# Performance work log

Measured on AMD Instinct MI355X. Metric: run time of the kernel, lower is better.

## Reference

```python
import jax, jax.numpy as jnp
import numpy as np

D_MODEL = 1024
D_STATE = 16
D_CONV = 4
EXPAND = 2
D_INNER = EXPAND * D_MODEL          # 2048
DT_RANK = D_MODEL // 16             # 64
B, L = 2, 1024
LN_EPS = 1e-5


def setup_inputs() -> dict:
    key = jax.random.key(0)
    ks = jax.random.split(key, 8)
    s = lambda k, shape, sc: jax.random.normal(k, shape, jnp.float32) * sc
    inp = {
        'x': jax.random.normal(ks[0], (B, L, D_MODEL), jnp.float32),
        'ln_w': jnp.ones((D_MODEL,), jnp.float32),
        'ln_b': jnp.zeros((D_MODEL,), jnp.float32),
        'W_in': s(ks[1], (2 * D_INNER, D_MODEL), 0.02),
        'conv_w': s(ks[2], (D_INNER, D_CONV), 0.1),
        'conv_b': jnp.zeros((D_INNER,), jnp.float32),
        'W_x': s(ks[3], (DT_RANK + 2 * D_STATE, D_INNER), 0.02),
        'W_dt': s(ks[4], (D_INNER, DT_RANK), 0.1),
        # softplus(-4.6) ~= 0.01 -> realistic small timestep init
        'b_dt': jnp.full((D_INNER,), -4.6, jnp.float32),
        # Mamba S4D-real init: A = [1..d_state] per channel
        'A_log': jnp.log(jnp.broadcast_to(
            jnp.arange(1, D_STATE + 1, dtype=jnp.float32), (D_INNER, D_STATE))),
        'Dp': jnp.ones((D_INNER,), jnp.float32),
        'W_out': s(ks[5], (D_MODEL, D_INNER), 0.02),
    }
    return inp


def _mamba_layer(x, ln_w, ln_b, W_in, conv_w, conv_b, W_x, W_dt, b_dt, A_log, Dp, W_out):
    # LayerNorm
    mu = x.mean(-1, keepdims=True)
    var = ((x - mu) ** 2).mean(-1, keepdims=True)
    xn = (x - mu) * jax.lax.rsqrt(var + LN_EPS) * ln_w + ln_b

    # in_proj -> (x_stream, gate z), each [B, L, D_INNER]
    xz = jnp.einsum('bld,ed->ble', xn, W_in)
    xs, z = jnp.split(xz, 2, axis=-1)

    # depthwise causal conv1d along L (kernel D_CONV) + SiLU
    xp = jnp.pad(xs, ((0, 0), (D_CONV - 1, 0), (0, 0)))
    conv = conv_b + sum(conv_w[:, k] * xp[:, k:k + L, :] for k in range(D_CONV))
    xs = jax.nn.silu(conv)

    # input-dependent dt, B, C
    xdbl = jnp.einsum('blc,ec->ble', xs, W_x)
    dt, Bm, Cm = jnp.split(xdbl, [DT_RANK, DT_RANK + D_STATE], axis=-1)
    dt = jax.nn.softplus(jnp.einsum('blr,cr->blc', dt, W_dt) + b_dt)  # [B,L,Din]

    # discretize: h_t = exp(dt*A) * h_{t-1} + (dt * B_t) * x_t
    A = -jnp.exp(A_log)                                  # [Din, N]
    dA = jnp.exp(dt[..., None] * A)                      # [B,L,Din,N]
    dBx = dt[..., None] * Bm[:, :, None, :] * xs[..., None]

    def comb(e1, e2):
        a1, b1 = e1
        a2, b2 = e2
        return a2 * a1, a2 * b1 + b2

    _, hs = jax.lax.associative_scan(comb, (dA, dBx), axis=1)  # [B,L,Din,N]

    y = jnp.einsum('blcn,bln->blc', hs, Cm) + Dp * xs
    y = y * jax.nn.silu(z)
    out = jnp.einsum('blc,dc->bld', y, W_out)
    # dropout in eval mode == identity; residual add
    return x + out


def reference(x, ln_w, ln_b, W_in, conv_w, conv_b, W_x, W_dt, b_dt, A_log, Dp, W_out):
    return _mamba_layer(x, ln_w, ln_b, W_in, conv_w, conv_b, W_x, W_dt, b_dt, A_log, Dp, W_out)
```

## Files before the change

### kernel.cpp

```cpp
#include <hip/hip_runtime.h>

typedef __bf16 bf16_t;
typedef __bf16 bf16x8 __attribute__((ext_vector_type(8)));
typedef __bf16 bf16x4 __attribute__((ext_vector_type(4)));
typedef float f32x4 __attribute__((ext_vector_type(4)));
typedef unsigned int u32;

#define NTOK 2048
#define LSEQ 1024
#define DMODEL 1024
#define DINNER 2048
#define NXD 96
#define DTRANK 64
#define NC 64
#define CL 16

__device__ __forceinline__ void gload16(const void* g, void* l) {
  __builtin_amdgcn_global_load_lds((const __attribute__((address_space(1))) u32*)g,
                                   (__attribute__((address_space(3))) u32*)l, 16, 0, 0);
}

#define CVT_N0 1048576
#define CVT_N1 (CVT_N0 + 49152)
#define CVT_N2 (CVT_N1 + 32768)
#define CVT_N3 (CVT_N2 + 524288)
__global__ __launch_bounds__(256) void k_cvt4(const float* __restrict__ a0, const float* __restrict__ a1,
                                              const float* __restrict__ a2, const float* __restrict__ a3,
                                              bf16_t* __restrict__ o0, bf16_t* __restrict__ o1,
                                              bf16_t* __restrict__ o2, bf16_t* __restrict__ o3) {
  int i = blockIdx.x * 256 + threadIdx.x;
  const float* src; bf16_t* dst; int idx;
  if (i < CVT_N0)      { src = a0; dst = o0; idx = i; }
  else if (i < CVT_N1) { src = a1; dst = o1; idx = i - CVT_N0; }
  else if (i < CVT_N2) { src = a2; dst = o2; idx = i - CVT_N1; }
  else if (i < CVT_N3) { src = a3; dst = o3; idx = i - CVT_N2; }
  else return;
  float4 v = reinterpret_cast<const float4*>(src)[idx];
  bf16x4 o = { (bf16_t)v.x, (bf16_t)v.y, (bf16_t)v.z, (bf16_t)v.w };
  reinterpret_cast<bf16x4*>(dst)[idx] = o;
}

__global__ __launch_bounds__(256) void k_ln(const float* __restrict__ x, const float* __restrict__ w,
                                            const float* __restrict__ b, bf16_t* __restrict__ xn) {
  const int row = blockIdx.x;
  const int tid = threadIdx.x;
  float4 v = reinterpret_cast<const float4*>(x + (size_t)row * DMODEL)[tid];
  float s = v.x + v.y + v.z + v.w;
  float q = v.x*v.x + v.y*v.y + v.z*v.z + v.w*v.w;
#pragma unroll
  for (int o = 32; o > 0; o >>= 1) { s += __shfl_down(s, o); q += __shfl_down(q, o); }
  __shared__ float sh[8];
  int wv = tid >> 6;
  if ((tid & 63) == 0) { sh[wv] = s; sh[4 + wv] = q; }
  __syncthreads();
  if (tid == 0) {
    sh[0] = sh[0] + sh[1] + sh[2] + sh[3];
    sh[4] = sh[4] + sh[5] + sh[6] + sh[7];
  }
  __syncthreads();
  float mu = sh[0] * (1.f / DMODEL);
  float var = sh[4] * (1.f / DMODEL) - mu * mu;
  float rs = rsqrtf(var + 1e-5f);
  float4 w4 = reinterpret_cast<const float4*>(w)[tid];
  float4 b4 = reinterpret_cast<const float4*>(b)[tid];
  bf16x4 o = { (bf16_t)((v.x - mu) * rs * w4.x + b4.x),
               (bf16_t)((v.y - mu) * rs * w4.y + b4.y),
               (bf16_t)((v.z - mu) * rs * w4.z + b4.z),
               (bf16_t)((v.w - mu) * rs * w4.w + b4.w) };
  reinterpret_cast<bf16x4*>(xn + (size_t)row * DMODEL)[tid] = o;
}

template <int BM, bool RESID, bool OUTBF>
__global__ __launch_bounds__(256) void k_gemm(const bf16_t* __restrict__ A, const bf16_t* __restrict__ Bt,
                                              void* __restrict__ Cout, const float* __restrict__ R,
                                              int N, int K) {
  constexpr int BN = 128;
  constexpr int MR = BM / 32;
  constexpr int NCHUNK = (BM + BN) * 4;
  constexpr int ITER = NCHUNK / 256;
  __shared__ bf16_t As[BM * 32];
  __shared__ bf16_t Bs[BN * 32];
  const int tid = threadIdx.x;
  const int w = tid >> 6, lane = tid & 63;

  const int nbx = gridDim.x;
  int nwg = gridDim.x * gridDim.y;
  int orig = blockIdx.y * gridDim.x + blockIdx.x;
  int cpx = nwg >> 3;
  int swz = (orig & 7) * cpx + (orig >> 3);
  int bx = swz % nbx, by = swz / nbx;
  const int brow = by * BM, bcol = bx * BN;
  const int wr = (w >> 1) * (BM / 2), wc = (w & 1) * 64;

  const bf16_t* gsrc[ITER];
  bf16_t* lbase[ITER];
#pragma unroll
  for (int i = 0; i < ITER; ++i) {
    int p0 = i * 256 + w * 64;
    int p = p0 + lane;
    if (p0 < BM * 4) {
      gsrc[i] = A + (size_t)(brow + (p >> 2)) * K + (p & 3) * 8;
      lbase[i] = &As[p0 * 8];
    } else {
      int q = p - BM * 4, q0 = p0 - BM * 4;
      gsrc[i] = Bt + (size_t)(bcol + (q >> 2)) * K + (q & 3) * 8;
      lbase[i] = &Bs[q0 * 8];
    }
  }

  f32x4 acc[MR][4] = {};
  for (int kk = 0; kk < K; kk += 32) {
    __syncthreads();
#pragma unroll
    for (int i = 0; i < ITER; ++i) gload16(gsrc[i] + kk, lbase[i]);
    __syncthreads();
    bf16x8 af[MR], bfr[4];
#pragma unroll
    for (int m = 0; m < MR; ++m)
      af[m] = *reinterpret_cast<const bf16x8*>(&As[(wr + m * 16 + (lane & 15)) * 32 + (lane >> 4) * 8]);
#pragma unroll
    for (int n = 0; n < 4; ++n)
      bfr[n] = *reinterpret_cast<const bf16x8*>(&Bs[(wc + n * 16 + (lane & 15)) * 32 + (lane >> 4) * 8]);
#pragma unroll
    for (int m = 0; m < MR; ++m)
#pragma unroll
      for (int n = 0; n < 4; ++n)
        acc[m][n] = __builtin_amdgcn_mfma_f32_16x16x32_bf16(af[m], bfr[n], acc[m][n], 0, 0, 0);
  }

#pragma unroll
  for (int m = 0; m < MR; ++m) {
#pragma unroll
    for (int n = 0; n < 4; ++n) {
      int col = bcol + wc + n * 16 + (lane & 15);
#pragma unroll
      for (int r = 0; r < 4; ++r) {
        int row = brow + wr + m * 16 + ((lane >> 4) << 2) + r;
        float v = acc[m][n][r];
        if (RESID) v += R[(size_t)row * N + col];
        if (OUTBF) ((bf16_t*)Cout)[(size_t)row * N + col] = (bf16_t)v;
        else       ((float*)Cout)[(size_t)row * N + col] = v;
      }
    }
  }
}

__global__ __launch_bounds__(256) void k_conv(const bf16_t* __restrict__ xz, const float* __restrict__ cw,
                                              const float* __restrict__ cb, float* __restrict__ xsf,
                                              bf16_t* __restrict__ xsB) {
  int gid = blockIdx.x * 256 + threadIdx.x;
  int c = gid & (DINNER - 1);
  int t = gid >> 11;
  int l = t & (LSEQ - 1);
  float4 w4 = reinterpret_cast<const float4*>(cw)[c];
  float wk[4] = { w4.x, w4.y, w4.z, w4.w };
  float v = cb[c];
#pragma unroll
  for (int k = 0; k < 4; ++k) {
    int ll = l + k - 3;
    if (ll >= 0) v += wk[k] * (float)xz[(size_t)(t + k - 3) * 4096 + c];
  }
  float sv = v / (1.f + __expf(-v));
  xsf[(size_t)t * DINNER + c] = sv;
  xsB[(size_t)t * DINNER + c] = (bf16_t)sv;
}

__global__ __launch_bounds__(256) void k_xproj(const bf16_t* __restrict__ A, const bf16_t* __restrict__ Bt,
                                               float* __restrict__ C) {
  __shared__ f32x4 red[4][6][64];
  int tid = threadIdx.x, w = tid >> 6, lane = tid & 63;
  int r0 = blockIdx.x * 16;
  int arow = r0 + (lane & 15);
  int kof = (lane >> 4) * 8;
  f32x4 acc[6] = {};
  for (int k = w * 512; k < (w + 1) * 512; k += 32) {
    bf16x8 af = *reinterpret_cast<const bf16x8*>(A + (size_t)arow * DINNER + k + kof);
#pragma unroll
    for (int j = 0; j < 6; ++j) {
      bf16x8 bfr = *reinterpret_cast<const bf16x8*>(Bt + (size_t)(j * 16 + (lane & 15)) * DINNER + k + kof);
      acc[j] = __builtin_amdgcn_mfma_f32_16x16x32_bf16(af, bfr, acc[j], 0, 0, 0);
    }
  }
#pragma unroll
  for (int j = 0; j < 6; ++j) red[w][j][lane] = acc[j];
  __syncthreads();
  for (int item = tid; item < 384; item += 256) {
    int j = item >> 6, li = item & 63;
    f32x4 s = red[0][j][li];
#pragma unroll
    for (int ww = 1; ww < 4; ++ww) s += red[ww][j][li];
    int col = j * 16 + (li & 15);
    int rowb = r0 + ((li >> 4) << 2);
#pragma unroll
    for (int r = 0; r < 4; ++r) C[(size_t)(rowb + r) * NXD + col] = s[r];
  }
}

__global__ __launch_bounds__(256) void k_dtproj(const float* __restrict__ xdbl, const bf16_t* __restrict__ Wdt,
                                                const float* __restrict__ bdt, float* __restrict__ dtf) {
  int tid = threadIdx.x, w = tid >> 6, lane = tid & 63;
  int r0 = blockIdx.y * 64 + w * 16;
  int c0 = blockIdx.x * 64;
  int arow = r0 + (lane & 15);
  int kof = (lane >> 4) * 8;
  f32x4 acc[4] = {};
#pragma unroll
  for (int ks = 0; ks < 2; ++ks) {
    int k = ks * 32;
    const float* ap = xdbl + (size_t)arow * NXD + k + kof;
    float4 a0 = *reinterpret_cast<const float4*>(ap);
    float4 a1 = *reinterpret_cast<const float4*>(ap + 4);
    bf16x8 af = { (bf16_t)a0.x, (bf16_t)a0.y, (bf16_t)a0.z, (bf16_t)a0.w,
                  (bf16_t)a1.x, (bf16_t)a1.y, (bf16_t)a1.z, (bf16_t)a1.w };
#pragma unroll
    for (int j = 0; j < 4; ++j) {
      bf16x8 bfr = *reinterpret_cast<const bf16x8*>(Wdt + (size_t)(c0 + j * 16 + (lane & 15)) * DTRANK + k + kof);
      acc[j] = __builtin_amdgcn_mfma_f32_16x16x32_bf16(af, bfr, acc[j], 0, 0, 0);
    }
  }
#pragma unroll
  for (int j = 0; j < 4; ++j) {
    int col = c0 + j * 16 + (lane & 15);
    float bb = bdt[col];
#pragma unroll
    for (int r = 0; r < 4; ++r) {
      int row = r0 + ((lane >> 4) << 2) + r;
      float v = acc[j][r] + bb;
      v = (v > 20.f) ? v : log1pf(__expf(v));
      dtf[(size_t)row * DINNER + col] = v;
    }
  }
}

__global__ __launch_bounds__(256) void k_scanA(const float* __restrict__ dtf, const float* __restrict__ xsf,
                                               const float* __restrict__ xdbl, const float* __restrict__ A_log,
                                               float* __restrict__ Sp, float* __restrict__ Ss) {
  int gid = blockIdx.x * 256 + threadIdx.x;
  int c = gid & (DINNER - 1);
  int chunk = (gid >> 11) & (NC - 1);
  int b = gid >> 17;
  int t0 = b * LSEQ + chunk * CL;
  float a[16];
#pragma unroll
  for (int n = 0; n < 16; n += 4) {
    float4 al = reinterpret_cast<const float4*>(A_log + (size_t)c * 16)[n >> 2];
    a[n] = -__expf(al.x); a[n + 1] = -__expf(al.y); a[n + 2] = -__expf(al.z); a[n + 3] = -__expf(al.w);
  }
  float ap[16], h[16];
#pragma unroll
  for (int n = 0; n < 16; ++n) { ap[n] = 1.f; h[n] = 0.f; }
#pragma unroll 4
  for (int l = 0; l < CL; ++l) {
    int t = t0 + l;
    float dt = dtf[(size_t)t * DINNER + c];
    float xv = xsf[(size_t)t * DINNER + c];
    float dtx = dt * xv;
    const float4* bp = reinterpret_cast<const float4*>(xdbl + (size_t)t * NXD + DTRANK);
    float4 b0 = bp[0], b1 = bp[1], b2 = bp[2], b3 = bp[3];
    float bv[16] = { b0.x, b0.y, b0.z, b0.w, b1.x, b1.y, b1.z, b1.w,
                     b2.x, b2.y, b2.z, b2.w, b3.x, b3.y, b3.z, b3.w };
#pragma unroll
    for (int n = 0; n < 16; ++n) {
      float e = __expf(dt * a[n]);
      ap[n] *= e;
      h[n] = e * h[n] + dtx * bv[n];
    }
  }
  size_t base = ((size_t)(b * NC + chunk) * 16) * DINNER + c;
#pragma unroll
  for (int n = 0; n < 16; ++n) {
    Sp[base + (size_t)n * DINNER] = ap[n];
    Ss[base + (size_t)n * DINNER] = h[n];
  }
}

__global__ __launch_bounds__(256) void k_scanB(const float* __restrict__ Sp, const float* __restrict__ Ss,
                                               float* __restrict__ Hi) {
  int gid = blockIdx.x * 256 + threadIdx.x;
  int c = gid & (DINNER - 1);
  int n = (gid >> 11) & 15;
  int b = gid >> 15;
  size_t idx = ((size_t)(b * NC) * 16 + n) * DINNER + c;
  const size_t stride = (size_t)16 * DINNER;
  float h = 0.f;
#pragma unroll 4
  for (int chunk = 0; chunk < NC; ++chunk) {
    Hi[idx] = h;
    h = Sp[idx] * h + Ss[idx];
    idx += stride;
  }
}

__global__ __launch_bounds__(256) void k_scanC(const float* __restrict__ dtf, const float* __restrict__ xsf,
                                               const float* __restrict__ xdbl, const float* __restrict__ A_log,
                                               const float* __restrict__ Hi, const float* __restrict__ Dp,
                                               const bf16_t* __restrict__ xz, bf16_t* __restrict__ yB) {
  int gid = blockIdx.x * 256 + threadIdx.x;
  int c = gid & (DINNER - 1);
  int chunk = (gid >> 11) & (NC - 1);
  int b = gid >> 17;
  int t0 = b * LSEQ + chunk * CL;
  float a[16];
#pragma unroll
  for (int n = 0; n < 16; n += 4) {
    float4 al = reinterpret_cast<const float4*>(A_log + (size_t)c * 16)[n >> 2];
    a[n] = -__expf(al.x); a[n + 1] = -__expf(al.y); a[n + 2] = -__expf(al.z); a[n + 3] = -__expf(al.w);
  }
  float h[16];
  size_t base = ((size_t)(b * NC + chunk) * 16) * DINNER + c;
#pragma unroll
  for (int n = 0; n < 16; ++n) h[n] = Hi[base + (size_t)n * DINNER];
  float dpc = Dp[c];
#pragma unroll 4
  for (int l = 0; l < CL; ++l) {
    int t = t0 + l;
    float dt = dtf[(size_t)t * DINNER + c];
    float xv = xsf[(size_t)t * DINNER + c];
    float zv = (float)xz[(size_t)t * 4096 + DINNER + c];
    float dtx = dt * xv;
    const float4* bp = reinterpret_cast<const float4*>(xdbl + (size_t)t * NXD + DTRANK);
    float4 b0 = bp[0], b1 = bp[1], b2 = bp[2], b3 = bp[3];
    float bv[16] = { b0.x, b0.y, b0.z, b0.w, b1.x, b1.y, b1.z, b1.w,
                     b2.x, b2.y, b2.z, b2.w, b3.x, b3.y, b3.z, b3.w };
    const float4* cp = reinterpret_cast<const float4*>(xdbl + (size_t)t * NXD + DTRANK + 16);
    float4 c0 = cp[0], c1 = cp[1], c2 = cp[2], c3 = cp[3];
    float cv[16] = { c0.x, c0.y, c0.z, c0.w, c1.x, c1.y, c1.z, c1.w,
                     c2.x, c2.y, c2.z, c2.w, c3.x, c3.y, c3.z, c3.w };
    float y = 0.f;
#pragma unroll
    for (int n = 0; n < 16; ++n) {
      float e = __expf(dt * a[n]);
      h[n] = e * h[n] + dtx * bv[n];
      y += h[n] * cv[n];
    }
    y += dpc * xv;
    y *= zv / (1.f + __expf(-zv));
    yB[(size_t)t * DINNER + c] = (bf16_t)y;
  }
}

extern "C" void kernel_launch(void* const* d_in, const int* in_sizes, int n_in,
                              void* d_out, int out_size, void* d_ws, size_t ws_size,
                              hipStream_t stream) {
  (void)in_sizes; (void)n_in; (void)out_size; (void)ws_size;
  const float* x      = (const float*)d_in[0];
  const float* ln_w   = (const float*)d_in[1];
  const float* ln_b   = (const float*)d_in[2];
  const float* W_in   = (const float*)d_in[3];
  const float* conv_w = (const float*)d_in[4];
  const float* conv_b = (const float*)d_in[5];
  const float* W_x    = (const float*)d_in[6];
  const float* W_dt   = (const float*)d_in[7];
  const float* b_dt   = (const float*)d_in[8];
  const float* A_log  = (const float*)d_in[9];
  const float* Dp     = (const float*)d_in[10];
  const float* W_out  = (const float*)d_in[11];
  float* out = (float*)d_out;

  char* ws = (char*)d_ws;
  size_t off = 0;
  auto alloc = [&](size_t bytes) { void* p = ws + off; off += (bytes + 255) & ~255ull; return p; };
  bf16_t* wInB  = (bf16_t*)alloc((size_t)4096 * 1024 * 2);
  bf16_t* wXB   = (bf16_t*)alloc((size_t)96 * 2048 * 2);
  bf16_t* wDtB  = (bf16_t*)alloc((size_t)2048 * 64 * 2);
  bf16_t* wOutB = (bf16_t*)alloc((size_t)1024 * 2048 * 2);
  bf16_t* xnB   = (bf16_t*)alloc((size_t)NTOK * DMODEL * 2);
  bf16_t* xzB   = (bf16_t*)alloc((size_t)NTOK * 4096 * 2);
  float*  xsf   = (float*)alloc((size_t)NTOK * DINNER * 4);
  bf16_t* xsB   = (bf16_t*)alloc((size_t)NTOK * DINNER * 2);
  float*  xdbl  = (float*)alloc((size_t)NTOK * NXD * 4);
  float*  dtf   = (float*)alloc((size_t)NTOK * DINNER * 4);
  float*  Sp    = (float*)alloc((size_t)2 * NC * 16 * DINNER * 4);
  float*  Ss    = (float*)alloc((size_t)2 * NC * 16 * DINNER * 4);
  float*  Hi    = (float*)alloc((size_t)2 * NC * 16 * DINNER * 4);
  bf16_t* yB    = (bf16_t*)alloc((size_t)NTOK * DINNER * 2);

  k_cvt4<<<(CVT_N3 + 255) / 256, 256, 0, stream>>>(W_in, W_x, W_dt, W_out, wInB, wXB, wDtB, wOutB);

  k_ln<<<NTOK, 256, 0, stream>>>(x, ln_w, ln_b, xnB);

  k_gemm<128, false, true><<<dim3(4096 / 128, NTOK / 128), 256, 0, stream>>>(xnB, wInB, xzB, nullptr, 4096, 1024);

  k_conv<<<NTOK * DINNER / 256, 256, 0, stream>>>(xzB, conv_w, conv_b, xsf, xsB);

  k_xproj<<<NTOK / 16, 256, 0, stream>>>(xsB, wXB, xdbl);

  k_dtproj<<<dim3(DINNER / 64, NTOK / 64), 256, 0, stream>>>(xdbl, wDtB, b_dt, dtf);

  k_scanA<<<2 * NC * DINNER / 256, 256, 0, stream>>>(dtf, xsf, xdbl, A_log, Sp, Ss);
  k_scanB<<<2 * 16 * DINNER / 256, 256, 0, stream>>>(Sp, Ss, Hi);
  k_scanC<<<2 * NC * DINNER / 256, 256, 0, stream>>>(dtf, xsf, xdbl, A_log, Hi, Dp, xzB, yB);

  k_gemm<64, true, false><<<dim3(1024 / 128, NTOK / 64), 256, 0, stream>>>(yB, wOutB, out, x, 1024, 2048);
}
```

Baseline: 280.1 us.

## XOR-swizzle GEMM LDS layout and split-K the out-projection with a reduction pass

Applies an XOR swizzle to the 16-byte chunks of each row in the A and B LDS tiles so that fragment reads hit different banks, removing LDS bank conflicts in both GEMMs. It also replaces the out-projection GEMM (64x128 tiles, K=2048) with a 128x128-tile split-K kernel over four K slices of 512. Each slice writes fp32 partials, and a separate kernel sums them and adds the residual. The split-K path raises the workgroup count and per-tile reuse, but adds a 32 MB partial buffer write and readback plus an extra launch.

```diff
diff --git a/kernel.cpp b/kernel.cpp
--- a/kernel.cpp
+++ b/kernel.cpp
@@ -70,6 +70,7 @@
   reinterpret_cast<bf16x4*>(xn + (size_t)row * DMODEL)[tid] = o;
 }
 
+
 template <int BM, bool RESID, bool OUTBF>
 __global__ __launch_bounds__(256) void k_gemm(const bf16_t* __restrict__ A, const bf16_t* __restrict__ Bt,
                                               void* __restrict__ Cout, const float* __restrict__ R,
@@ -99,12 +100,14 @@
     int p0 = i * 256 + w * 64;
     int p = p0 + lane;
     if (p0 < BM * 4) {
-      gsrc[i] = A + (size_t)(brow + (p >> 2)) * K + (p & 3) * 8;
+      int r = p >> 2, s = (p & 3) ^ ((r >> 2) & 3);
+      gsrc[i] = A + (size_t)(brow + r) * K + s * 8;
       lbase[i] = &As[p0 * 8];
     } else {
-      int q = p - BM * 4, q0 = p0 - BM * 4;
-      gsrc[i] = Bt + (size_t)(bcol + (q >> 2)) * K + (q & 3) * 8;
-      lbase[i] = &Bs[q0 * 8];
+      int q = p - BM * 4;
+      int r = q >> 2, s = (q & 3) ^ ((r >> 2) & 3);
+      gsrc[i] = Bt + (size_t)(bcol + r) * K + s * 8;
+      lbase[i] = &Bs[(p0 - BM * 4) * 8];
     }
   }
 
@@ -116,11 +119,15 @@
     __syncthreads();
     bf16x8 af[MR], bfr[4];
 #pragma unroll
-    for (int m = 0; m < MR; ++m)
-      af[m] = *reinterpret_cast<const bf16x8*>(&As[(wr + m * 16 + (lane & 15)) * 32 + (lane >> 4) * 8]);
-#pragma unroll
-    for (int n = 0; n < 4; ++n)
-      bfr[n] = *reinterpret_cast<const bf16x8*>(&Bs[(wc + n * 16 + (lane & 15)) * 32 + (lane >> 4) * 8]);
+    for (int m = 0; m < MR; ++m) {
+      int rr = wr + m * 16 + (lane & 15);
+      af[m] = *reinterpret_cast<const bf16x8*>(&As[rr * 32 + (((lane >> 4) ^ ((rr >> 2) & 3)) << 3)]);
+    }
+#pragma unroll
+    for (int n = 0; n < 4; ++n) {
+      int rc = wc + n * 16 + (lane & 15);
+      bfr[n] = *reinterpret_cast<const bf16x8*>(&Bs[rc * 32 + (((lane >> 4) ^ ((rc >> 2) & 3)) << 3)]);
+    }
 #pragma unroll
     for (int m = 0; m < MR; ++m)
 #pragma unroll
@@ -143,6 +150,95 @@
       }
     }
   }
+}
+
+__global__ __launch_bounds__(256) void k_gemmsk(const bf16_t* __restrict__ A, const bf16_t* __restrict__ Bt,
+                                                float* __restrict__ P) {
+  constexpr int BM = 128, BN = 128, K = 2048, N = 1024, KSP = 512;
+  __shared__ bf16_t As[BM * 32];
+  __shared__ bf16_t Bs[BN * 32];
+  const int tid = threadIdx.x, w = tid >> 6, lane = tid & 63;
+  const int nbx = gridDim.x;
+  int nwg = gridDim.x * gridDim.y;
+  int orig = blockIdx.y * gridDim.x + blockIdx.x;
+  int cpx = nwg >> 3;
+  int swz = (orig & 7) * cpx + (orig >> 3);
+  int bx = swz % nbx, byf = swz / nbx;
+  const int split = byf & 3, by = byf >> 2;
+  const int brow = by * BM, bcol = bx * BN;
+  const int wr = (w >> 1) * 64, wc = (w & 1) * 64;
+  const int k0 = split * KSP;
+
+  const bf16_t* gsrc[4];
+  bf16_t* lbase[4];
+#pragma unroll
+  for (int i = 0; i < 4; ++i) {
+    int p0 = i * 256 + w * 64;
+    int p = p0 + lane;
+    if (p0 < BM * 4) {
+      int r = p >> 2, s = (p & 3) ^ ((r >> 2) & 3);
+      gsrc[i] = A + (size_t)(brow + r) * K + s * 8;
+      lbase[i] = &As[p0 * 8];
+    } else {
+      int q = p - BM * 4;
+      int r = q >> 2, s = (q & 3) ^ ((r >> 2) & 3);
+      gsrc[i] = Bt + (size_t)(bcol + r) * K + s * 8;
+      lbase[i] = &Bs[(p0 - BM * 4) * 8];
+    }
+  }
+
+  f32x4 acc[4][4] = {};
+  for (int kk = k0; kk < k0 + KSP; kk += 32) {
+    __syncthreads();
+#pragma unroll
+    for (int i = 0; i < 4; ++i) gload16(gsrc[i] + kk, lbase[i]);
+    __syncthreads();
+    bf16x8 af[4], bfr[4];
+#pragma unroll
+    for (int m = 0; m < 4; ++m) {
+      int rr = wr + m * 16 + (lane & 15);
+      af[m] = *reinterpret_cast<const bf16x8*>(&As[rr * 32 + (((lane >> 4) ^ ((rr >> 2) & 3)) << 3)]);
+    }
+#pragma unroll
+    for (int n = 0; n < 4; ++n) {
+      int rc = wc + n * 16 + (lane & 15);
+      bfr[n] = *reinterpret_cast<const bf16x8*>(&Bs[rc * 32 + (((lane >> 4) ^ ((rc >> 2) & 3)) << 3)]);
+    }
+#pragma unroll
+    for (int m = 0; m < 4; ++m)
+#pragma unroll
+      for (int n = 0; n < 4; ++n)
+        acc[m][n] = __builtin_amdgcn_mfma_f32_16x16x32_bf16(af[m], bfr[n], acc[m][n], 0, 0, 0);
+  }
+
+  float* Pp = P + (size_t)split * ((size_t)NTOK * N);
+#pragma unroll
+  for (int m = 0; m < 4; ++m)
+#pragma unroll
+    for (int n = 0; n < 4; ++n) {
+      int col = bcol + wc + n * 16 + (lane & 15);
+#pragma unroll
+      for (int r = 0; r < 4; ++r) {
+        int row = brow + wr + m * 16 + ((lane >> 4) << 2) + r;
+        Pp[(size_t)row * N + col] = acc[m][n][r];
+      }
+    }
+}
+
+__global__ __launch_bounds__(256) void k_red(const float* __restrict__ P, const float* __restrict__ x,
+                                             float* __restrict__ out) {
+  int i = blockIdx.x * 256 + threadIdx.x;
+  constexpr size_t S = (size_t)NTOK * 1024 / 4;
+  float4 a = reinterpret_cast<const float4*>(P)[i];
+  float4 b = reinterpret_cast<const float4*>(P)[i + S];
+  float4 c = reinterpret_cast<const float4*>(P)[i + 2 * S];
+  float4 d = reinterpret_cast<const float4*>(P)[i + 3 * S];
+  float4 xv = reinterpret_cast<const float4*>(x)[i];
+  float4 o = { a.x + b.x + c.x + d.x + xv.x,
+               a.y + b.y + c.y + d.y + xv.y,
+               a.z + b.z + c.z + d.z + xv.z,
+               a.w + b.w + c.w + d.w + xv.w };
+  reinterpret_cast<float4*>(out)[i] = o;
 }
 
 __global__ __launch_bounds__(256) void k_conv(const bf16_t* __restrict__ xz, const float* __restrict__ cw,
@@ -374,6 +470,7 @@
   float*  Ss    = (float*)alloc((size_t)2 * NC * 16 * DINNER * 4);
   float*  Hi    = (float*)alloc((size_t)2 * NC * 16 * DINNER * 4);
   bf16_t* yB    = (bf16_t*)alloc((size_t)NTOK * DINNER * 2);
+  float*  Pq    = (float*)alloc((size_t)4 * NTOK * 1024 * 4);
 
   k_cvt4<<<(CVT_N3 + 255) / 256, 256, 0, stream>>>(W_in, W_x, W_dt, W_out, wInB, wXB, wDtB, wOutB);
 
@@ -391,5 +488,6 @@
   k_scanB<<<2 * 16 * DINNER / 256, 256, 0, stream>>>(Sp, Ss, Hi);
   k_scanC<<<2 * NC * DINNER / 256, 256, 0, stream>>>(dtf, xsf, xdbl, A_log, Hi, Dp, xzB, yB);
 
-  k_gemm<64, true, false><<<dim3(1024 / 128, NTOK / 64), 256, 0, stream>>>(yB, wOutB, out, x, 1024, 2048);
-}
+  k_gemmsk<<<dim3(8, 64), 256, 0, stream>>>(yB, wOutB, Pq);
+  k_red<<<NTOK * 1024 / 4 / 256, 256, 0, stream>>>(Pq, x, out);
+}
```

Result: faster. 271.5 us (-3.1%).
